# Kernel optimization log

Hardware: AMD Instinct MI355X
Metric: run time of the kernel (lower is better)

The kernel has to match this reference:

```python
import jax, jax.numpy as jnp
from jax import lax
import numpy as np

B, T, D, H, C = 64, 256, 1024, 1024, 27


def _lstm_layer(x, Wih, Whh, bih, bhh):
    """Batch-first LSTM layer matching torch.nn.LSTM gate math.
    x: (N, S, Din) -> returns hs: (N, S, H). Gate order: i, f, g, o."""
    N = x.shape[0]
    Hh = Whh.shape[1]
    # precompute input contribution for all steps: (N, S, 4H)
    xg = jnp.einsum('nsd,gd->nsg', x, Wih) + bih + bhh

    def step(carry, xg_t):
        h, c = carry
        g = xg_t + h @ Whh.T  # (N, 4H)
        i, f, gg, o = jnp.split(g, 4, axis=-1)
        c = jax.nn.sigmoid(f) * c + jax.nn.sigmoid(i) * jnp.tanh(gg)
        h = jax.nn.sigmoid(o) * jnp.tanh(c)
        return (h, c), h

    h0 = jnp.zeros((N, Hh), x.dtype)
    (_, _), hs = lax.scan(step, (h0, h0), jnp.swapaxes(xg, 0, 1))  # scan over S
    return jnp.swapaxes(hs, 0, 1)  # (N, S, H)


def setup_inputs() -> dict:
    key = jax.random.key(0)
    ks = jax.random.split(key, 13)
    s = 1.0 / np.sqrt(H)
    u = lambda k, shape: jax.random.uniform(k, shape, jnp.float32, -s, s)
    return {
        'x': jax.random.normal(ks[0], (B, T, D), jnp.float32),
        'Wih0': u(ks[1], (4 * H, D)), 'Whh0': u(ks[2], (4 * H, H)),
        'bih0': u(ks[3], (4 * H,)), 'bhh0': u(ks[4], (4 * H,)),
        'Wih1': u(ks[5], (4 * H, H)), 'Whh1': u(ks[6], (4 * H, H)),
        'bih1': u(ks[7], (4 * H,)), 'bhh1': u(ks[8], (4 * H,)),
        'W1': u(ks[9], (H // 2, H)), 'b1': u(ks[10], (H // 2,)),
        'W2': u(ks[11], (C, H // 2)), 'b2': u(ks[12], (C,)),
    }


def reference(x, Wih0, Whh0, bih0, bhh0, Wih1, Whh1, bih1, bhh1, W1, b1, W2, b2):
    # Original module permutes (B,T,D) -> (T,B,D) but the LSTM is batch_first,
    # so it treats T as batch and recurs over the original batch axis B.
    xp = jnp.transpose(x, (1, 0, 2))           # (T, B, D): batch=T, seq=B
    h1 = _lstm_layer(xp, Wih0, Whh0, bih0, bhh0)  # (T, B, H)
    h2 = _lstm_layer(h1, Wih1, Whh1, bih1, bhh1)  # (T, B, H)
    out = h2[-1]                                # (B, H): last 'batch' row
    fc = jax.nn.relu(out @ W1.T + b1)
    return fc @ W2.T + b2                       # (B, C)
```

## Files before the change

kernel.cpp:

```cpp
#include <hip/hip_runtime.h>
#include <math.h>


#define NBLK 256
#define TPB  512
#define HDIM 1024
#define SEQ  64
#define GUARD (1L << 20)
#define POISON 0xAAAAAAAAu
#define ENCOFF 0x55555555u

#define WS_H1 0
#define WS_H2 (SEQ * HDIM)
#define WS_FCB (2 * SEQ * HDIM)

#define FMA4(A, W, Hv)                                                         \
  (A).x = fmaf((W).x, (Hv).x, (A).x);                                          \
  (A).y = fmaf((W).y, (Hv).y, (A).y);                                          \
  (A).z = fmaf((W).z, (Hv).z, (A).z);                                          \
  (A).w = fmaf((W).w, (Hv).w, (A).w)

__device__ __forceinline__ float sigmoidf_(float v) {
  return 1.0f / (1.0f + expf(-v));
}
__device__ __forceinline__ float hsum4(float4 a) {
  return (a.x + a.y) + (a.z + a.w);
}
__device__ __forceinline__ float wave_sum(float v) {
#pragma unroll
  for (int m = 32; m >= 1; m >>= 1) v += __shfl_xor(v, m, 64);
  return v;
}

__device__ __forceinline__ void st_u32(unsigned* p, unsigned v) {
  __hip_atomic_store(p, v, __ATOMIC_RELAXED, __HIP_MEMORY_SCOPE_AGENT);
}
__device__ __forceinline__ unsigned enc(float v) {
  return __float_as_uint(v) + ENCOFF;
}
__device__ __forceinline__ float dec(unsigned u) {
  return __uint_as_float(u - ENCOFF);
}
__device__ __forceinline__ float2 poll2(const unsigned* p) {
  const unsigned long long* pp = (const unsigned long long*)p;
  unsigned lo, hi;
  long g = 0;
  for (;;) {
    unsigned long long u =
        __hip_atomic_load(pp, __ATOMIC_RELAXED, __HIP_MEMORY_SCOPE_AGENT);
    lo = (unsigned)u;
    hi = (unsigned)(u >> 32);
    if ((lo != POISON) & (hi != POISON)) break;
    __builtin_amdgcn_s_sleep(1);
    if (++g > GUARD) break;
  }
  asm volatile("" ::: "memory");
  return make_float2(dec(lo), dec(hi));
}

__global__ void __launch_bounds__(TPB, 2) lstm_persist(
    const float* __restrict__ x,
    const float* __restrict__ Wih0, const float* __restrict__ Whh0,
    const float* __restrict__ bih0, const float* __restrict__ bhh0,
    const float* __restrict__ Wih1, const float* __restrict__ Whh1,
    const float* __restrict__ bih1, const float* __restrict__ bhh1,
    const float* __restrict__ W1, const float* __restrict__ b1,
    const float* __restrict__ W2, const float* __restrict__ b2,
    float* __restrict__ out, unsigned* ws) {
  __shared__ float sA[2][HDIM];
  __shared__ float sB[2][HDIM];
  __shared__ float sX[2][HDIM];

  unsigned* h1dat = ws + WS_H1;
  unsigned* h2dat = ws + WS_H2;
  unsigned* fcb = ws + WS_FCB;

  const int tid = threadIdx.x;
  const int b = blockIdx.x;
  const int lane = tid & 63;
  const int q = tid >> 6;
  const int L = q >> 2;
  const int elem = (b << 2) + (q & 3);

  const float* Wih = L ? Wih1 : Wih0;
  const float* Whh = L ? Whh1 : Whh0;
  const float* bi = L ? bih1 : bih0;
  const float* bh = L ? bhh1 : bhh0;

  float4 wi[4][4], wr[4][4];
  float bias[4];
#pragma unroll
  for (int g = 0; g < 4; ++g) {
    const int row = (g << 10) + elem;
    bias[g] = bi[row] + bh[row];
    const float4* pi = (const float4*)(Wih + (size_t)row * HDIM);
    const float4* pr = (const float4*)(Whh + (size_t)row * HDIM);
#pragma unroll
    for (int k = 0; k < 4; ++k) {
      wi[g][k] = pi[(k << 6) + lane];
      wr[g][k] = pr[(k << 6) + lane];
    }
  }

  float cell = 0.0f;

  for (int p = 0; p <= SEQ; ++p) {
    const int pb = p & 1;
    float2 xv = make_float2(0, 0);
    if (p < SEQ)
      xv = ((const float2*)x)[(size_t)(p * 256 + 255) * 512 + tid];
    float2 vb = make_float2(0, 0);
    if (p >= 2) vb = poll2(h2dat + (size_t)(p - 2) * HDIM + (tid << 1));
    float2 va = make_float2(0, 0);
    if (p >= 1) va = poll2(h1dat + (size_t)(p - 1) * HDIM + (tid << 1));

    ((float2*)sA[pb])[tid] = va;
    ((float2*)sB[pb])[tid] = vb;
    ((float2*)sX[pb])[tid] = xv;
    __syncthreads();

    const float4* A4 = (const float4*)sA[pb];
    const float4* B4 = (const float4*)sB[pb];
    const float4* X4 = (const float4*)sX[pb];

    if (L == 0) {
      if (p < SEQ) {
        float4 acc[4];
#pragma unroll
        for (int g = 0; g < 4; ++g) acc[g] = make_float4(0, 0, 0, 0);
#pragma unroll
        for (int k = 0; k < 4; ++k) {
          float4 xf = X4[(k << 6) + lane];
          float4 hf = A4[(k << 6) + lane];
#pragma unroll
          for (int g = 0; g < 4; ++g) {
            FMA4(acc[g], wi[g][k], xf);
            FMA4(acc[g], wr[g][k], hf);
          }
        }
        float gi = wave_sum(hsum4(acc[0])) + bias[0];
        float gf = wave_sum(hsum4(acc[1])) + bias[1];
        float gg = wave_sum(hsum4(acc[2])) + bias[2];
        float go = wave_sum(hsum4(acc[3])) + bias[3];
        cell = sigmoidf_(gf) * cell + sigmoidf_(gi) * tanhf(gg);
        float hv = sigmoidf_(go) * tanhf(cell);
        if (lane == 0) st_u32(h1dat + (size_t)p * HDIM + elem, enc(hv));
      }
    } else {
      if (p >= 1) {
        float4 acc[4];
#pragma unroll
        for (int g = 0; g < 4; ++g) acc[g] = make_float4(0, 0, 0, 0);
#pragma unroll
        for (int k = 0; k < 4; ++k) {
          float4 iv = A4[(k << 6) + lane];
          float4 hf = B4[(k << 6) + lane];
#pragma unroll
          for (int g = 0; g < 4; ++g) {
            FMA4(acc[g], wi[g][k], iv);
            FMA4(acc[g], wr[g][k], hf);
          }
        }
        float gi = wave_sum(hsum4(acc[0])) + bias[0];
        float gf = wave_sum(hsum4(acc[1])) + bias[1];
        float gg = wave_sum(hsum4(acc[2])) + bias[2];
        float go = wave_sum(hsum4(acc[3])) + bias[3];
        cell = sigmoidf_(gf) * cell + sigmoidf_(gi) * tanhf(gg);
        float hv = sigmoidf_(go) * tanhf(cell);
        if (lane == 0) st_u32(h2dat + (size_t)(p - 1) * HDIM + elem, enc(hv));
      }
    }
  }

  __syncthreads();
  {
    const int s = b >> 2, ch = b & 3;
    float2 v = poll2(h2dat + (size_t)s * HDIM + (tid << 1));
    ((float2*)sA[0])[tid] = v;
    __syncthreads();
    const float4* A4 = (const float4*)sA[0];
    for (int t = 0; t < 16; ++t) {
      const int j = (ch << 7) + (q << 4) + t;
      const float4* w4 = (const float4*)(W1 + (size_t)j * HDIM);
      float4 acc = make_float4(0, 0, 0, 0);
#pragma unroll
      for (int k = 0; k < 4; ++k) {
        float4 wv = w4[(k << 6) + lane];
        float4 hv = A4[(k << 6) + lane];
        FMA4(acc, wv, hv);
      }
      float v2 = wave_sum(hsum4(acc));
      if (lane == 0)
        st_u32(fcb + (size_t)s * 512 + j, enc(fmaxf(v2 + b1[j], 0.0f)));
    }
  }

  if (b < 64) {
    if (tid < 256) {
      float2 v = poll2(fcb + (size_t)b * 512 + (tid << 1));
      ((float2*)sB[0])[tid] = v;
    }
    __syncthreads();
    const float4* B4v = (const float4*)sB[0];
    for (int c = q; c < 27; c += 8) {
      const float4* w4 = (const float4*)(W2 + (size_t)c * 512);
      float4 acc = make_float4(0, 0, 0, 0);
#pragma unroll
      for (int k = 0; k < 2; ++k) {
        float4 wv = w4[(k << 6) + lane];
        float4 hv = B4v[(k << 6) + lane];
        FMA4(acc, wv, hv);
      }
      float v = wave_sum(hsum4(acc));
      if (lane == 0) out[b * 27 + c] = v + b2[c];
    }
  }
}

extern "C" void kernel_launch(void* const* d_in, const int* in_sizes, int n_in,
                              void* d_out, int out_size, void* d_ws,
                              size_t ws_size, hipStream_t stream) {
  (void)in_sizes; (void)n_in; (void)out_size; (void)ws_size;
  const float* x    = (const float*)d_in[0];
  const float* Wih0 = (const float*)d_in[1];
  const float* Whh0 = (const float*)d_in[2];
  const float* bih0 = (const float*)d_in[3];
  const float* bhh0 = (const float*)d_in[4];
  const float* Wih1 = (const float*)d_in[5];
  const float* Whh1 = (const float*)d_in[6];
  const float* bih1 = (const float*)d_in[7];
  const float* bhh1 = (const float*)d_in[8];
  const float* W1   = (const float*)d_in[9];
  const float* b1   = (const float*)d_in[10];
  const float* W2   = (const float*)d_in[11];
  const float* b2   = (const float*)d_in[12];
  float* out = (float*)d_out;
  unsigned* ws = (unsigned*)d_ws;

  hipLaunchKernelGGL(lstm_persist, dim3(NBLK), dim3(TPB), 0, stream, x, Wih0,
                     Whh0, bih0, bhh0, Wih1, Whh1, bih1, bhh1, W1, b1, W2, b2,
                     out, ws);
}
```

Before: 425.0 us.

## Replicate hidden-state broadcast buffers so block groups poll separate copies

Each produced hidden value is now written to up to eight replicated workspace chains, one per lane, and each block polls only the replica chosen by its block index. The aim is to spread the polling traffic of all 256 blocks across several memory locations so fewer blocks contend on the same cache lines. In exchange every step does more atomic stores and uses more workspace, and the replica count is picked at launch from the available workspace size.

Measured after the change: 394.2 us. 7.2% less time.

```diff
diff --git a/kernel.cpp b/kernel.cpp
--- a/kernel.cpp
+++ b/kernel.cpp
@@ -6,19 +6,18 @@
 #define TPB  512
 #define HDIM 1024
 #define SEQ  64
+#define CHAIN (SEQ * HDIM)
 #define GUARD (1L << 20)
 #define POISON 0xAAAAAAAAu
 #define ENCOFF 0x55555555u
 
-#define WS_H1 0
-#define WS_H2 (SEQ * HDIM)
-#define WS_FCB (2 * SEQ * HDIM)
-
 #define FMA4(A, W, Hv)                                                         \
-  (A).x = fmaf((W).x, (Hv).x, (A).x);                                          \
-  (A).y = fmaf((W).y, (Hv).y, (A).y);                                          \
-  (A).z = fmaf((W).z, (Hv).z, (A).z);                                          \
-  (A).w = fmaf((W).w, (Hv).w, (A).w)
+  do {                                                                         \
+    (A).x = fmaf((W).x, (Hv).x, (A).x);                                        \
+    (A).y = fmaf((W).y, (Hv).y, (A).y);                                        \
+    (A).z = fmaf((W).z, (Hv).z, (A).z);                                        \
+    (A).w = fmaf((W).w, (Hv).w, (A).w);                                        \
+  } while (0)
 
 __device__ __forceinline__ float sigmoidf_(float v) {
   return 1.0f / (1.0f + expf(-v));
@@ -66,14 +65,14 @@
     const float* __restrict__ bih1, const float* __restrict__ bhh1,
     const float* __restrict__ W1, const float* __restrict__ b1,
     const float* __restrict__ W2, const float* __restrict__ b2,
-    float* __restrict__ out, unsigned* ws) {
+    float* __restrict__ out, unsigned* ws, int nrep) {
   __shared__ float sA[2][HDIM];
   __shared__ float sB[2][HDIM];
   __shared__ float sX[2][HDIM];
 
-  unsigned* h1dat = ws + WS_H1;
-  unsigned* h2dat = ws + WS_H2;
-  unsigned* fcb = ws + WS_FCB;
+  unsigned* h1rep = ws;
+  unsigned* h2rep = ws + (size_t)nrep * CHAIN;
+  unsigned* fcb = ws + 2ull * (size_t)nrep * CHAIN;
 
   const int tid = threadIdx.x;
   const int b = blockIdx.x;
@@ -82,6 +81,10 @@
   const int L = q >> 2;
   const int elem = (b << 2) + (q & 3);
 
+  const int rep = b & (nrep - 1);
+  unsigned* h1r = h1rep + (size_t)rep * CHAIN;
+  unsigned* h2r = h2rep + (size_t)rep * CHAIN;
+
   const float* Wih = L ? Wih1 : Wih0;
   const float* Whh = L ? Whh1 : Whh0;
   const float* bi = L ? bih1 : bih0;
@@ -110,9 +113,9 @@
     if (p < SEQ)
       xv = ((const float2*)x)[(size_t)(p * 256 + 255) * 512 + tid];
     float2 vb = make_float2(0, 0);
-    if (p >= 2) vb = poll2(h2dat + (size_t)(p - 2) * HDIM + (tid << 1));
+    if (p >= 2) vb = poll2(h2r + (size_t)(p - 2) * HDIM + (tid << 1));
     float2 va = make_float2(0, 0);
-    if (p >= 1) va = poll2(h1dat + (size_t)(p - 1) * HDIM + (tid << 1));
+    if (p >= 1) va = poll2(h1r + (size_t)(p - 1) * HDIM + (tid << 1));
 
     ((float2*)sA[pb])[tid] = va;
     ((float2*)sB[pb])[tid] = vb;
@@ -144,7 +147,9 @@
         float go = wave_sum(hsum4(acc[3])) + bias[3];
         cell = sigmoidf_(gf) * cell + sigmoidf_(gi) * tanhf(gg);
         float hv = sigmoidf_(go) * tanhf(cell);
-        if (lane == 0) st_u32(h1dat + (size_t)p * HDIM + elem, enc(hv));
+        if (lane < nrep)
+          st_u32(h1rep + (size_t)lane * CHAIN + (size_t)p * HDIM + elem,
+                 enc(hv));
       }
     } else {
       if (p >= 1) {
@@ -167,7 +172,9 @@
         float go = wave_sum(hsum4(acc[3])) + bias[3];
         cell = sigmoidf_(gf) * cell + sigmoidf_(gi) * tanhf(gg);
         float hv = sigmoidf_(go) * tanhf(cell);
-        if (lane == 0) st_u32(h2dat + (size_t)(p - 1) * HDIM + elem, enc(hv));
+        if (lane < nrep)
+          st_u32(h2rep + (size_t)lane * CHAIN + (size_t)(p - 1) * HDIM + elem,
+                 enc(hv));
       }
     }
   }
@@ -175,7 +182,7 @@
   __syncthreads();
   {
     const int s = b >> 2, ch = b & 3;
-    float2 v = poll2(h2dat + (size_t)s * HDIM + (tid << 1));
+    float2 v = poll2(h2r + (size_t)s * HDIM + (tid << 1));
     ((float2*)sA[0])[tid] = v;
     __syncthreads();
     const float4* A4 = (const float4*)sA[0];
@@ -220,7 +227,7 @@
 extern "C" void kernel_launch(void* const* d_in, const int* in_sizes, int n_in,
                               void* d_out, int out_size, void* d_ws,
                               size_t ws_size, hipStream_t stream) {
-  (void)in_sizes; (void)n_in; (void)out_size; (void)ws_size;
+  (void)in_sizes; (void)n_in; (void)out_size;
   const float* x    = (const float*)d_in[0];
   const float* Wih0 = (const float*)d_in[1];
   const float* Whh0 = (const float*)d_in[2];
@@ -237,7 +244,13 @@
   float* out = (float*)d_out;
   unsigned* ws = (unsigned*)d_ws;
 
+  int nrep = 1;
+  for (int r = 8; r >= 1; r >>= 1) {
+    size_t need = (2ull * (size_t)r * CHAIN + (size_t)SEQ * 512) * 4ull;
+    if (need <= ws_size) { nrep = r; break; }
+  }
+
   hipLaunchKernelGGL(lstm_persist, dim3(NBLK), dim3(TPB), 0, stream, x, Wih0,
                      Whh0, bih0, bhh0, Wih1, Whh1, bih1, bhh1, W1, b1, W2, b2,
-                     out, ws);
-}
+                     out, ws, nrep);
+}
```
